# Kernel optimization log

Measured on AMD Instinct MI355X. Metric: run time of the kernel, lower is better.

The kernel has to match this reference:

```python
import jax, jax.numpy as jnp
import numpy as np

VOCAB = 32000
D_IN = 1024      # == 2 * N_OUT so highway uses raw x (k=3 SRU path)
N_OUT = 512      # hidden per direction
N_LAYERS = 4
L, B = 1024, 16


def _sru_bidir_layer(x, W, b, n):
    """x: (L,B,2n), W: (2n, 6n) [dir0: xt,f,r | dir1: xt,f,r], b: (4n,) = [bf(2n), br(2n)]."""
    u = jnp.einsum('lbd,dk->lbk', x, W)  # (L,B,6n)
    bf, br = b[:2 * n], b[2 * n:]
    hs, cs = [], []
    for d, rev in ((0, False), (1, True)):
        ud = u[..., d * 3 * n:(d + 1) * 3 * n]
        xt = ud[..., :n]
        f = jax.nn.sigmoid(ud[..., n:2 * n] + bf[d * n:(d + 1) * n])
        r = jax.nn.sigmoid(ud[..., 2 * n:3 * n] + br[d * n:(d + 1) * n])
        xp = x[..., d * n:(d + 1) * n]  # highway input (k=3 case)

        def step(c, inp):
            xt_t, f_t, r_t, xp_t = inp
            c = f_t * c + (1.0 - f_t) * xt_t
            h = r_t * jnp.tanh(c) + (1.0 - r_t) * xp_t
            return c, h

        c0 = jnp.zeros((x.shape[1], n), x.dtype)
        c_last, h = jax.lax.scan(step, c0, (xt, f, r, xp), reverse=rev)
        hs.append(h)
        cs.append(c_last)
    return jnp.concatenate(hs, -1), jnp.concatenate(cs, -1)


def setup_inputs() -> dict:
    key = jax.random.key(0)
    k1, k2, k3, k4 = jax.random.split(key, 4)
    rnn_input = jax.random.randint(k1, (L, B), 0, VOCAB, dtype=jnp.int32)
    input_lengths = jax.random.randint(k2, (B,), 1, L + 1, dtype=jnp.int32)
    emb = jax.random.normal(k3, (VOCAB, D_IN), dtype=jnp.float32) * 0.05
    scale = 1.0 / np.sqrt(D_IN)
    Ws = jax.random.normal(k4, (N_LAYERS, D_IN, 6 * N_OUT), dtype=jnp.float32) * scale
    bs = jnp.zeros((N_LAYERS, 4 * N_OUT), dtype=jnp.float32)
    return {"rnn_input": rnn_input, "input_lengths": input_lengths,
            "emb": emb, "Ws": Ws, "bs": bs}


def reference(rnn_input, input_lengths, emb, Ws, bs):
    # input_lengths is unused in the original forward (no packing applied to SRU input)
    n = Ws.shape[-1] // 6
    x = emb[rnn_input]  # (L,B,D_IN)
    c_finals = []
    for l in range(Ws.shape[0]):
        x, c = _sru_bidir_layer(x, Ws[l], bs[l], n)
        c_finals.append(c)
    hidden = jnp.stack(c_finals, 0)  # (N_LAYERS, B, 2n)
    return x, hidden
```

## Files before the change

kernel.cpp:

```cpp
#include <hip/hip_runtime.h>
#include <hip/hip_bf16.h>
#include <cmath>

#define L_SEQ  1024
#define BATCH  16
#define NOUT   512
#define DIN    1024
#define NBIG   3072
#define NLAYERS 4
#define NTOK   (L_SEQ * BATCH)
#define NCHAIN 16384
#define SEG    32
#define SEGLEN (L_SEQ / SEG)

typedef __attribute__((ext_vector_type(8))) short bf16x8;
typedef __attribute__((ext_vector_type(4))) float f32x4;

__device__ __forceinline__ unsigned short f2bf(float f) {
    unsigned x = __float_as_uint(f);
    unsigned r = (x + 0x7fffu + ((x >> 16) & 1u)) >> 16;
    return (unsigned short)r;
}
__device__ __forceinline__ float bf2f(unsigned short hv) {
    return __uint_as_float((unsigned)hv << 16);
}
__device__ __forceinline__ float sigmf(float v) {
    return 1.f / (1.f + __expf(-v));
}
__device__ __forceinline__ void async16(const void* g, const void* l) {
    __builtin_amdgcn_global_load_lds(
        (const __attribute__((address_space(1))) unsigned int*)g,
        (__attribute__((address_space(3))) unsigned int*)l, 16, 0, 0);
}

__global__ __launch_bounds__(256)
void transpose_w(const float* __restrict__ Ws, unsigned short* __restrict__ Wt) {
    __shared__ float tile[32][33];
    int l = blockIdx.z;
    const float* W = Ws + (size_t)l * DIN * NBIG;
    unsigned short* Wo = Wt + (size_t)l * NBIG * DIN;
    int n0 = blockIdx.x * 32, k0 = blockIdx.y * 32;
    int tx = threadIdx.x & 31, ty = threadIdx.x >> 5;
    #pragma unroll
    for (int i = 0; i < 4; i++)
        tile[ty + 8 * i][tx] = W[(size_t)(k0 + ty + 8 * i) * NBIG + n0 + tx];
    __syncthreads();
    #pragma unroll
    for (int i = 0; i < 4; i++)
        Wo[(size_t)(n0 + ty + 8 * i) * DIN + k0 + tx] = f2bf(tile[tx][ty + 8 * i]);
}

__global__ void embed_kernel(const int* __restrict__ tok,
                             const float* __restrict__ emb,
                             float* __restrict__ x,
                             unsigned short* __restrict__ xbf) {
    int t = blockIdx.x;
    int row = tok[t];
    float4 v = ((const float4*)(emb + (size_t)row * DIN))[threadIdx.x];
    ((float4*)(x + (size_t)t * DIN))[threadIdx.x] = v;
    ushort4 h;
    h.x = f2bf(v.x); h.y = f2bf(v.y); h.z = f2bf(v.z); h.w = f2bf(v.w);
    ((ushort4*)(xbf + (size_t)t * DIN))[threadIdx.x] = h;
}

__global__ __launch_bounds__(256)
void gemm_bf16(const unsigned short* __restrict__ Abf,
               const unsigned short* __restrict__ Bt,
               unsigned short* __restrict__ u_xt,
               unsigned short* __restrict__ u_f,
               unsigned short* __restrict__ u_r) {
    __shared__ __align__(16) unsigned short As[128 * 64];
    __shared__ __align__(16) unsigned short Bs[128 * 64];

    const int tid  = threadIdx.x;
    const int lane = tid & 63;
    const int w    = tid >> 6;
    const int wm   = w & 1, wn = w >> 1;
    const int quad = lane >> 4, l16 = lane & 15;

    const int M0 = blockIdx.y * 128;
    const int N0 = blockIdx.x * 128;

    f32x4 acc[4][4];
    #pragma unroll
    for (int i = 0; i < 4; i++)
        #pragma unroll
        for (int j = 0; j < 4; j++)
            acc[i][j] = (f32x4){0.f, 0.f, 0.f, 0.f};

    const int sr = lane >> 3;
    const int sc = (lane & 7) ^ sr;

    for (int k0 = 0; k0 < DIN; k0 += 64) {
        #pragma unroll
        for (int g = 0; g < 4; g++) {
            int rbase = w * 32 + g * 8;
            int r = rbase + sr;
            async16(Abf + (size_t)(M0 + r) * DIN + k0 + sc * 8, &As[rbase * 64]);
            async16(Bt  + (size_t)(N0 + r) * DIN + k0 + sc * 8, &Bs[rbase * 64]);
        }
        __syncthreads();

        #pragma unroll
        for (int s = 0; s < 2; s++) {
            bf16x8 af[4], bg[4];
            #pragma unroll
            for (int t = 0; t < 4; t++) {
                int ra = wm * 64 + t * 16 + l16;
                int sa = (s * 4 + quad) ^ (ra & 7);
                af[t] = *(const bf16x8*)&As[ra * 64 + sa * 8];
                int rb = wn * 64 + t * 16 + l16;
                int sb = (s * 4 + quad) ^ (rb & 7);
                bg[t] = *(const bf16x8*)&Bs[rb * 64 + sb * 8];
            }
            #pragma unroll
            for (int i = 0; i < 4; i++)
                #pragma unroll
                for (int j = 0; j < 4; j++)
                    acc[i][j] = __builtin_amdgcn_mfma_f32_16x16x32_bf16(af[i], bg[j], acc[i][j], 0, 0, 0);
        }
        __syncthreads();
    }

    #pragma unroll
    for (int i = 0; i < 4; i++) {
        int gm = M0 + wm * 64 + i * 16 + quad * 4;
        #pragma unroll
        for (int j = 0; j < 4; j++) {
            int gn = N0 + wn * 64 + j * 16 + l16;
            int dir  = gn >= 3 * NOUT;
            int jj   = gn - dir * 3 * NOUT;
            int plane = jj >> 9;
            int feat  = jj & 511;
            unsigned short* p = (plane == 0 ? u_xt : plane == 1 ? u_f : u_r)
                                + (size_t)gm * DIN + dir * NOUT + feat;
            #pragma unroll
            for (int r = 0; r < 4; r++) p[(size_t)r * DIN] = f2bf(acc[i][j][r]);
        }
    }
}


__global__ __launch_bounds__(256)
void scan_phaseA(const unsigned short* __restrict__ u_xt, const unsigned short* __restrict__ u_f,
                 const float* __restrict__ bias,
                 float* __restrict__ Aseg, float* __restrict__ Bseg) {
    int g = blockIdx.x * 256 + threadIdx.x;
    int chain = g & (NCHAIN - 1);
    int s = g >> 14;
    int rest = chain & 1023;
    float bf = bias[rest];

    int d = rest >> 9;
    int t0 = d ? (L_SEQ - 1 - s * SEGLEN) : (s * SEGLEN);
    int sgn = d ? -1 : 1;
    long long idx = (long long)t0 * NCHAIN + chain;
    long long step = (long long)sgn * NCHAIN;

    float c = 0.f, A = 1.f;
    #pragma unroll 8
    for (int j = 0; j < SEGLEN; j++) {
        float xt = bf2f(u_xt[idx]);
        float f = sigmf(bf2f(u_f[idx]) + bf);
        c = f * c + (1.f - f) * xt;
        A *= f;
        idx += step;
    }
    Aseg[g] = A;
    Bseg[g] = c;
}

__global__ __launch_bounds__(256)
void scan_phaseB(const float* __restrict__ Aseg, const float* __restrict__ Bseg,
                 float* __restrict__ cstart, float* __restrict__ c_out) {
    int chain = blockIdx.x * 256 + threadIdx.x;
    float c = 0.f;
    #pragma unroll
    for (int s = 0; s < SEG; s++) {
        int g = s * NCHAIN + chain;
        cstart[g] = c;
        c = Aseg[g] * c + Bseg[g];
    }
    c_out[chain] = c;
}

__global__ __launch_bounds__(256)
void scan_phaseC(const unsigned short* __restrict__ u_xt, const unsigned short* __restrict__ u_f,
                 const unsigned short* __restrict__ u_r,
                 float* __restrict__ x, unsigned short* __restrict__ xbf,
                 const float* __restrict__ bias, const float* __restrict__ cstart,
                 int write_bf) {
    int g = blockIdx.x * 256 + threadIdx.x;
    int chain = g & (NCHAIN - 1);
    int s = g >> 14;
    int rest = chain & 1023;
    float bf = bias[rest];
    float br = bias[1024 + rest];

    int d = rest >> 9;
    int t0 = d ? (L_SEQ - 1 - s * SEGLEN) : (s * SEGLEN);
    int sgn = d ? -1 : 1;
    long long idx = (long long)t0 * NCHAIN + chain;
    long long step = (long long)sgn * NCHAIN;

    float c = cstart[g];
    #pragma unroll 4
    for (int j = 0; j < SEGLEN; j++) {
        float xt = bf2f(u_xt[idx]);
        float f = sigmf(bf2f(u_f[idx]) + bf);
        float r = sigmf(bf2f(u_r[idx]) + br);
        float xp = x[idx];
        c = f * c + (1.f - f) * xt;
        float th = 1.f - 2.f / (__expf(2.f * c) + 1.f);
        float h = r * th + (1.f - r) * xp;
        x[idx] = h;
        if (write_bf) xbf[idx] = f2bf(h);
        idx += step;
    }
}

extern "C" void kernel_launch(void* const* d_in, const int* in_sizes, int n_in,
                              void* d_out, int out_size, void* d_ws, size_t ws_size,
                              hipStream_t stream) {
    const int*   tok = (const int*)d_in[0];
    const float* emb = (const float*)d_in[2];
    const float* Ws  = (const float*)d_in[3];
    const float* bs  = (const float*)d_in[4];

    float* out    = (float*)d_out;
    float* x      = out;
    float* hidden = out + (size_t)NTOK * DIN;

    char* ws = (char*)d_ws;
    unsigned short* u_xt   = (unsigned short*)ws;
    unsigned short* u_f    = (unsigned short*)(ws + (32u  << 20));
    unsigned short* u_r    = (unsigned short*)(ws + (64u  << 20));
    unsigned short* xbf    = (unsigned short*)(ws + (96u  << 20));
    unsigned short* Wt     = (unsigned short*)(ws + (128u << 20));
    float*          Aseg   = (float*)(ws + (152u << 20));
    float*          Bseg   = (float*)(ws + (154u << 20));
    float*          cstart = (float*)(ws + (156u << 20));

    transpose_w<<<dim3(NBIG / 32, DIN / 32, NLAYERS), 256, 0, stream>>>(Ws, Wt);
    embed_kernel<<<NTOK, 256, 0, stream>>>(tok, emb, x, xbf);

    const int scan_blocks = NCHAIN * SEG / 256;

    for (int l = 0; l < NLAYERS; l++) {
        const unsigned short* Wl = Wt + (size_t)l * NBIG * DIN;
        const float* b = bs + (size_t)l * 4 * NOUT;
        gemm_bf16<<<dim3(NBIG / 128, NTOK / 128), 256, 0, stream>>>(xbf, Wl, u_xt, u_f, u_r);
        scan_phaseA<<<scan_blocks, 256, 0, stream>>>(u_xt, u_f, b, Aseg, Bseg);
        scan_phaseB<<<NCHAIN / 256, 256, 0, stream>>>(Aseg, Bseg, cstart,
                                                      hidden + (size_t)l * BATCH * DIN);
        scan_phaseC<<<scan_blocks, 256, 0, stream>>>(u_xt, u_f, u_r, x, xbf, b, cstart,
                                                     l < NLAYERS - 1);
    }
}
```

Baseline: 961.0 us.

## Vectorize scan phases to 8 chains per thread and double segment count

Scan phases A and C now handle 8 adjacent chains per thread with 16-byte vector loads and stores of bf16 gates, fp32 state and outputs, instead of one scalar element per thread. The segment count rises from 32 to 64 so the grid stays large enough after the per-thread work grows eightfold, and the workspace offsets for the segment buffers are widened to fit. The aim is to cut memory instruction count and make better use of bandwidth in the memory-bound scan kernels, at the cost of more registers per thread and a longer serial combine in phase B.

New measurement: 990.5 us. 3.1% more time.

```diff
diff --git a/kernel.cpp b/kernel.cpp
--- a/kernel.cpp
+++ b/kernel.cpp
@@ -10,10 +10,12 @@
 #define NLAYERS 4
 #define NTOK   (L_SEQ * BATCH)
 #define NCHAIN 16384
-#define SEG    32
+#define SEG    64
 #define SEGLEN (L_SEQ / SEG)
+#define VEC    8
 
 typedef __attribute__((ext_vector_type(8))) short bf16x8;
+typedef __attribute__((ext_vector_type(8))) unsigned short u16x8;
 typedef __attribute__((ext_vector_type(4))) float f32x4;
 
 __device__ __forceinline__ unsigned short f2bf(float f) {
@@ -146,28 +148,41 @@
                  const float* __restrict__ bias,
                  float* __restrict__ Aseg, float* __restrict__ Bseg) {
     int g = blockIdx.x * 256 + threadIdx.x;
-    int chain = g & (NCHAIN - 1);
-    int s = g >> 14;
-    int rest = chain & 1023;
-    float bf = bias[rest];
-
+    int grp = g & (NCHAIN / VEC - 1);
+    int s = g >> 11;
+    int cb = grp * VEC;
+    int rest = cb & 1023;
     int d = rest >> 9;
+
+    float4 b0 = *(const float4*)(bias + rest);
+    float4 b1 = *(const float4*)(bias + rest + 4);
+    float bfv[8] = {b0.x, b0.y, b0.z, b0.w, b1.x, b1.y, b1.z, b1.w};
+
     int t0 = d ? (L_SEQ - 1 - s * SEGLEN) : (s * SEGLEN);
-    int sgn = d ? -1 : 1;
-    long long idx = (long long)t0 * NCHAIN + chain;
-    long long step = (long long)sgn * NCHAIN;
-
-    float c = 0.f, A = 1.f;
-    #pragma unroll 8
+    int idx = t0 * NCHAIN + cb;
+    int step = d ? -NCHAIN : NCHAIN;
+
+    float c[8], A[8];
+    #pragma unroll
+    for (int k = 0; k < 8; k++) { c[k] = 0.f; A[k] = 1.f; }
+
+    #pragma unroll 4
     for (int j = 0; j < SEGLEN; j++) {
-        float xt = bf2f(u_xt[idx]);
-        float f = sigmf(bf2f(u_f[idx]) + bf);
-        c = f * c + (1.f - f) * xt;
-        A *= f;
+        u16x8 xt8 = *(const u16x8*)(u_xt + idx);
+        u16x8 f8  = *(const u16x8*)(u_f + idx);
+        #pragma unroll
+        for (int k = 0; k < 8; k++) {
+            float f = sigmf(bf2f(f8[k]) + bfv[k]);
+            c[k] = f * c[k] + (1.f - f) * bf2f(xt8[k]);
+            A[k] *= f;
+        }
         idx += step;
     }
-    Aseg[g] = A;
-    Bseg[g] = c;
+    int og = s * NCHAIN + cb;
+    *(float4*)(Aseg + og)     = make_float4(A[0], A[1], A[2], A[3]);
+    *(float4*)(Aseg + og + 4) = make_float4(A[4], A[5], A[6], A[7]);
+    *(float4*)(Bseg + og)     = make_float4(c[0], c[1], c[2], c[3]);
+    *(float4*)(Bseg + og + 4) = make_float4(c[4], c[5], c[6], c[7]);
 }
 
 __global__ __launch_bounds__(256)
@@ -175,7 +190,7 @@
                  float* __restrict__ cstart, float* __restrict__ c_out) {
     int chain = blockIdx.x * 256 + threadIdx.x;
     float c = 0.f;
-    #pragma unroll
+    #pragma unroll 8
     for (int s = 0; s < SEG; s++) {
         int g = s * NCHAIN + chain;
         cstart[g] = c;
@@ -191,30 +206,53 @@
                  const float* __restrict__ bias, const float* __restrict__ cstart,
                  int write_bf) {
     int g = blockIdx.x * 256 + threadIdx.x;
-    int chain = g & (NCHAIN - 1);
-    int s = g >> 14;
-    int rest = chain & 1023;
-    float bf = bias[rest];
-    float br = bias[1024 + rest];
-
+    int grp = g & (NCHAIN / VEC - 1);
+    int s = g >> 11;
+    int cb = grp * VEC;
+    int rest = cb & 1023;
     int d = rest >> 9;
+
+    float4 b0 = *(const float4*)(bias + rest);
+    float4 b1 = *(const float4*)(bias + rest + 4);
+    float bfv[8] = {b0.x, b0.y, b0.z, b0.w, b1.x, b1.y, b1.z, b1.w};
+    float4 r0 = *(const float4*)(bias + 1024 + rest);
+    float4 r1 = *(const float4*)(bias + 1024 + rest + 4);
+    float brv[8] = {r0.x, r0.y, r0.z, r0.w, r1.x, r1.y, r1.z, r1.w};
+
     int t0 = d ? (L_SEQ - 1 - s * SEGLEN) : (s * SEGLEN);
-    int sgn = d ? -1 : 1;
-    long long idx = (long long)t0 * NCHAIN + chain;
-    long long step = (long long)sgn * NCHAIN;
-
-    float c = cstart[g];
-    #pragma unroll 4
+    int idx = t0 * NCHAIN + cb;
+    int step = d ? -NCHAIN : NCHAIN;
+
+    int og = s * NCHAIN + cb;
+    float4 c0 = *(const float4*)(cstart + og);
+    float4 c1 = *(const float4*)(cstart + og + 4);
+    float c[8] = {c0.x, c0.y, c0.z, c0.w, c1.x, c1.y, c1.z, c1.w};
+
+    #pragma unroll 2
     for (int j = 0; j < SEGLEN; j++) {
-        float xt = bf2f(u_xt[idx]);
-        float f = sigmf(bf2f(u_f[idx]) + bf);
-        float r = sigmf(bf2f(u_r[idx]) + br);
-        float xp = x[idx];
-        c = f * c + (1.f - f) * xt;
-        float th = 1.f - 2.f / (__expf(2.f * c) + 1.f);
-        float h = r * th + (1.f - r) * xp;
-        x[idx] = h;
-        if (write_bf) xbf[idx] = f2bf(h);
+        u16x8 xt8 = *(const u16x8*)(u_xt + idx);
+        u16x8 f8  = *(const u16x8*)(u_f + idx);
+        u16x8 rr8 = *(const u16x8*)(u_r + idx);
+        float4 xp0 = *(const float4*)(x + idx);
+        float4 xp1 = *(const float4*)(x + idx + 4);
+        float xp[8] = {xp0.x, xp0.y, xp0.z, xp0.w, xp1.x, xp1.y, xp1.z, xp1.w};
+        float h[8];
+        #pragma unroll
+        for (int k = 0; k < 8; k++) {
+            float f = sigmf(bf2f(f8[k]) + bfv[k]);
+            float r = sigmf(bf2f(rr8[k]) + brv[k]);
+            c[k] = f * c[k] + (1.f - f) * bf2f(xt8[k]);
+            float th = 1.f - 2.f / (__expf(2.f * c[k]) + 1.f);
+            h[k] = r * th + (1.f - r) * xp[k];
+        }
+        *(float4*)(x + idx)     = make_float4(h[0], h[1], h[2], h[3]);
+        *(float4*)(x + idx + 4) = make_float4(h[4], h[5], h[6], h[7]);
+        if (write_bf) {
+            u16x8 hb;
+            #pragma unroll
+            for (int k = 0; k < 8; k++) hb[k] = f2bf(h[k]);
+            *(u16x8*)(xbf + idx) = hb;
+        }
         idx += step;
     }
 }
@@ -238,13 +276,13 @@
     unsigned short* xbf    = (unsigned short*)(ws + (96u  << 20));
     unsigned short* Wt     = (unsigned short*)(ws + (128u << 20));
     float*          Aseg   = (float*)(ws + (152u << 20));
-    float*          Bseg   = (float*)(ws + (154u << 20));
-    float*          cstart = (float*)(ws + (156u << 20));
+    float*          Bseg   = (float*)(ws + (156u << 20));
+    float*          cstart = (float*)(ws + (160u << 20));
 
     transpose_w<<<dim3(NBIG / 32, DIN / 32, NLAYERS), 256, 0, stream>>>(Ws, Wt);
     embed_kernel<<<NTOK, 256, 0, stream>>>(tok, emb, x, xbf);
 
-    const int scan_blocks = NCHAIN * SEG / 256;
+    const int scan_blocks = NCHAIN / VEC * SEG / 256;
 
     for (int l = 0; l < NLAYERS; l++) {
         const unsigned short* Wl = Wt + (size_t)l * NBIG * DIN;
```
